# Kernel optimization log

Hardware: AMD Instinct MI355X
Metric: run time of the kernel (lower is better)

Reference implementation:

```python
import jax, jax.numpy as jnp
import numpy as np

N_USER = 50000
N_ITEM = 100000
D = 64            # embed_size; layer_size = [64, 64, 64]
NL = 3            # number of propagation layers
NNZ = 2400000     # nonzeros of sparse Laplacian L
B = 1024          # batch of (user, pos_item, neg_item)
N = N_USER + N_ITEM


def setup_inputs() -> dict:
    key = jax.random.key(0)
    ks = jax.random.split(key, 20)
    inp = {}
    # learned parameters
    inp["user_emb"] = jax.random.normal(ks[0], (N_USER, D), jnp.float32) * 0.1
    inp["item_emb"] = jax.random.normal(ks[1], (N_ITEM, D), jnp.float32) * 0.1
    inp["lin1_w"] = jax.random.normal(ks[2], (4, D // 2), jnp.float32) * 0.5
    inp["lin1_b"] = jnp.zeros((D // 2,), jnp.float32)
    inp["lin2_w"] = jax.random.normal(ks[3], (D // 2, D), jnp.float32) * 0.2
    inp["lin2_b"] = jnp.zeros((D,), jnp.float32)
    inp["w1"] = jax.random.normal(ks[4], (NL, D, D), jnp.float32) * (1.0 / np.sqrt(D))
    inp["b1"] = jnp.zeros((NL, D), jnp.float32)
    inp["w2"] = jax.random.normal(ks[5], (NL, D, D), jnp.float32) * (1.0 / np.sqrt(D))
    inp["b2"] = jnp.zeros((NL, D), jnp.float32)
    # sparse normalized Laplacian L in COO form (eye_mat handled as +E)
    inp["lap_row"] = jax.random.randint(ks[6], (NNZ,), 0, N, jnp.int32)
    inp["lap_col"] = jax.random.randint(ks[7], (NNZ,), 0, N, jnp.int32)
    inp["lap_val"] = jax.random.uniform(ks[8], (NNZ,), jnp.float32) * (1.0 / 16.0)
    # forward args
    inp["user_idx"] = jax.random.randint(ks[9], (B,), 0, N_USER, jnp.int32)
    inp["user_feat"] = jax.random.normal(ks[10], (B, 4), jnp.float32)
    inp["pos_idx"] = jax.random.randint(ks[11], (B,), 0, N_ITEM, jnp.int32)
    inp["neg_idx"] = jax.random.randint(ks[12], (B,), 0, N_ITEM, jnp.int32)
    inp["mlp_ratio"] = jnp.float32(0.5)
    return inp


def reference(user_emb, item_emb, user_feat, lin1_w, lin1_b, lin2_w, lin2_b,
              w1, b1, w2, b2, lap_val, mlp_ratio,
              lap_row, lap_col, user_idx, pos_idx, neg_idx):
    n_user = user_emb.shape[0]
    n_nodes = user_emb.shape[0] + item_emb.shape[0]

    # user MLP: two stacked Linears (no activation in between, per Sequential)
    user_mlp = (user_feat @ lin1_w + lin1_b) @ lin2_w + lin2_b  # [B, D]
    # in-place no_grad embedding blend (stop_gradient mirrors torch.no_grad on mlp path)
    upd = user_emb[user_idx] * (1.0 - mlp_ratio) + jax.lax.stop_gradient(user_mlp) * mlp_ratio
    ue = user_emb.at[user_idx].set(upd)

    E = jnp.concatenate([ue, item_emb], axis=0)  # [N, D]

    def spmm(X):
        # L @ X via gather-multiply-segment_sum over COO nonzeros
        return jax.ops.segment_sum(lap_val[:, None] * X[lap_col], lap_row,
                                   num_segments=n_nodes)

    all_E = [E]
    for k in range(w1.shape[0]):
        L_E = spmm(E)                 # L @ E
        L_I_E = L_E + E               # (L + I) @ E
        msg = (L_I_E @ w1[k] + b1[k]) + ((L_E * E) @ w2[k] + b2[k])
        E = jax.nn.leaky_relu(msg, negative_slope=0.2)
        # F.normalize(E, p=2, dim=1) with eps=1e-12
        norm = E / jnp.maximum(jnp.linalg.norm(E, axis=1, keepdims=True), 1e-12)
        all_E.append(norm)

    all_E = jnp.concatenate(all_E, axis=1)  # [N, D*(NL+1)]
    users = all_E[:n_user]
    items = all_E[n_user:]
    return (users[user_idx], items[pos_idx], items[neg_idx])
```

## Files before the change

kernel.cpp:

```cpp
#include <hip/hip_runtime.h>
#include <hip/hip_bf16.h>

#define N_USERC 50000
#define N_ITEMC 100000
#define NNODE   150000
#define DIM     64
#define NLAYERS 3
#define NNZC    2400000
#define BATCH   1024

#define RPB     128
#define NBUCK   1172
#define NCHUNK  512
#define CHUNK   4688
#define CAPB    3072

using short8 = __attribute__((ext_vector_type(8))) short;
using f32x4  = __attribute__((ext_vector_type(4))) float;

__device__ __forceinline__ float bf2f(ushort u) {
    return __uint_as_float(((unsigned)u) << 16);
}
__device__ __forceinline__ ushort f2bf(float f) {
    unsigned u = __float_as_uint(f);
    u += 0x7FFF + ((u >> 16) & 1);
    return (ushort)(u >> 16);
}

__device__ __forceinline__ int block_excl_scan(int v, int* lds) {
    int lane = threadIdx.x & 63;
    int wid  = threadIdx.x >> 6;
    int nw   = (blockDim.x + 63) >> 6;
    int inc = v;
#pragma unroll
    for (int o = 1; o < 64; o <<= 1) {
        int n = __shfl_up(inc, o, 64);
        if (lane >= o) inc += n;
    }
    if (lane == 63) lds[wid] = inc;
    __syncthreads();
    if (wid == 0) {
        int tv = (lane < nw) ? lds[lane] : 0;
#pragma unroll
        for (int o = 1; o < 16; o <<= 1) {
            int n = __shfl_up(tv, o, 64);
            if (lane >= o) tv += n;
        }
        if (lane < nw) lds[lane] = tv;
    }
    __syncthreads();
    int woff = (wid == 0) ? 0 : lds[wid - 1];
    return woff + (inc - v);
}

__global__ void k_copy_E(const float* __restrict__ ue, const float* __restrict__ ie,
                         ushort* __restrict__ Ebf) {
    int i = blockIdx.x * blockDim.x + threadIdx.x;
    const int userEnd = N_USERC * DIM / 4;
    const int total   = NNODE * DIM / 4;
    if (i < total) {
        float4 v;
        if (i < userEnd) v = ((const float4*)ue)[i];
        else             v = ((const float4*)ie)[i - userEnd];
        ushort4 b;
        b.x = f2bf(v.x); b.y = f2bf(v.y); b.z = f2bf(v.z); b.w = f2bf(v.w);
        ((ushort4*)Ebf)[i] = b;
    }
}

__global__ void k_winner(const int* __restrict__ user_idx, int* __restrict__ winner) {
    int b = blockIdx.x * blockDim.x + threadIdx.x;
    if (b < BATCH) atomicMax(&winner[user_idx[b]], b);
}

__global__ void k_mlp_update(const float* __restrict__ user_emb,
                             const float* __restrict__ user_feat,
                             const float* __restrict__ l1w, const float* __restrict__ l1b,
                             const float* __restrict__ l2w, const float* __restrict__ l2b,
                             const float* __restrict__ ratio_p,
                             const int* __restrict__ user_idx,
                             const int* __restrict__ winner,
                             ushort* __restrict__ Ebf) {
    int b = blockIdx.x;
    int d = threadIdx.x;
    int u = user_idx[b];
    if (winner[u] != b) return;
    float ratio = ratio_p[0];
    float uf0 = user_feat[b * 4 + 0], uf1 = user_feat[b * 4 + 1];
    float uf2 = user_feat[b * 4 + 2], uf3 = user_feat[b * 4 + 3];
    float acc = l2b[d];
#pragma unroll
    for (int j = 0; j < 32; ++j) {
        float h = l1b[j] + uf0 * l1w[0 * 32 + j] + uf1 * l1w[1 * 32 + j]
                         + uf2 * l1w[2 * 32 + j] + uf3 * l1w[3 * 32 + j];
        acc += h * l2w[j * DIM + d];
    }
    float v = user_emb[u * DIM + d] * (1.f - ratio) + acc * ratio;
    Ebf[u * DIM + d] = f2bf(v);
}

__global__ void k_prepW(const float* __restrict__ w1, const float* __restrict__ w2,
                        ushort* __restrict__ Wtg) {
    int i = blockIdx.x * blockDim.x + threadIdx.x;
    if (i >= NLAYERS * 64 * 128) return;
    int layer = i >> 13;
    int rem = i & 8191;
    int n = rem >> 7, kk = rem & 127;
    float v = (kk < 64) ? w1[layer * 4096 + kk * 64 + n]
                        : w2[layer * 4096 + (kk - 64) * 64 + n];
    Wtg[i] = f2bf(v);
}

__global__ __launch_bounds__(256) void k_chunksort(const int* __restrict__ rows,
                                                   const int* __restrict__ cols,
                                                   const float* __restrict__ vals,
                                                   unsigned long long* __restrict__ tmp,
                                                   ushort* __restrict__ scanus) {
    __shared__ int hist[NBUCK];
    __shared__ int sutil[16];
    __shared__ unsigned long long stag[CHUNK];

    const int c = blockIdx.x;
    const int s = c * CHUNK;
    const int e = (s + CHUNK < NNZC) ? s + CHUNK : NNZC;
    const int t = threadIdx.x;

    for (int i = t; i < NBUCK; i += 256) hist[i] = 0;
    __syncthreads();
    for (int i = s + t; i < e; i += 256) atomicAdd(&hist[rows[i] >> 7], 1);
    __syncthreads();

    int loc[5];
    int sum = 0;
#pragma unroll
    for (int k = 0; k < 5; ++k) {
        int idx = t * 5 + k;
        int v = (idx < NBUCK) ? hist[idx] : 0;
        loc[k] = sum;
        sum += v;
    }
    int excl = block_excl_scan(sum, sutil);
#pragma unroll
    for (int k = 0; k < 5; ++k) {
        int idx = t * 5 + k;
        if (idx < NBUCK) hist[idx] = excl + loc[k];
    }
    __syncthreads();

    for (int i = t; i < NBUCK; i += 256) scanus[(size_t)c * (NBUCK + 1) + i] = (ushort)hist[i];
    if (t == 0) scanus[(size_t)c * (NBUCK + 1) + NBUCK] = (ushort)(e - s);
    __syncthreads();

    for (int i = s + t; i < e; i += 256) {
        int r = rows[i];
        int b = r >> 7, ro = r & 127;
        unsigned hi = ((unsigned)ro << 18) | (unsigned)cols[i];
        unsigned long long pk = ((unsigned long long)hi << 32) | (unsigned)__float_as_uint(vals[i]);
        int pos = atomicAdd(&hist[b], 1);
        stag[pos] = pk;
    }
    __syncthreads();

    int n = e - s;
    for (int i = t; i < n; i += 256) tmp[s + i] = stag[i];
}

__global__ void k_buckcnt(const ushort* __restrict__ scanus, int* __restrict__ bcnt) {
    int b = blockIdx.x * blockDim.x + threadIdx.x;
    if (b >= NBUCK) return;
    int sum = 0;
    for (int c = 0; c < NCHUNK; ++c) {
        const ushort* row = scanus + (size_t)c * (NBUCK + 1);
        sum += (int)row[b + 1] - (int)row[b];
    }
    bcnt[b] = sum;
}

__global__ __launch_bounds__(256) void k_bscan(const int* __restrict__ bcnt,
                                               int* __restrict__ bstart,
                                               int* __restrict__ rowptr) {
    __shared__ int sutil[16];
    int t = threadIdx.x;
    int loc[5];
    int sum = 0;
#pragma unroll
    for (int k = 0; k < 5; ++k) {
        int idx = t * 5 + k;
        int v = (idx < NBUCK) ? bcnt[idx] : 0;
        loc[k] = sum;
        sum += v;
    }
    int excl = block_excl_scan(sum, sutil);
#pragma unroll
    for (int k = 0; k < 5; ++k) {
        int idx = t * 5 + k;
        if (idx < NBUCK) bstart[idx] = excl + loc[k];
    }
    if (t == 0) { bstart[NBUCK] = NNZC; rowptr[NNODE] = NNZC; }
}

__global__ __launch_bounds__(256) void k_compact(const ushort* __restrict__ scanus,
                                                 const int* __restrict__ bstart,
                                                 const unsigned long long* __restrict__ tmp,
                                                 unsigned long long* __restrict__ csr,
                                                 int* __restrict__ rowptr) {
    __shared__ int runstart[NCHUNK];
    __shared__ int pref[NCHUNK + 1];
    __shared__ int sutil[16];
    __shared__ int rcur[RPB];
    __shared__ unsigned long long stag[CAPB];
    const int b = blockIdx.x;
    const int t = threadIdx.x;

    for (int r = t; r < NCHUNK; r += 256) {
        const ushort* row = scanus + (size_t)r * (NBUCK + 1);
        int s0 = row[b], s1 = row[b + 1];
        runstart[r] = r * CHUNK + s0;
        pref[r] = s1 - s0;
    }
    if (t < RPB) rcur[t] = 0;
    __syncthreads();
    int v0 = pref[t * 2], v1 = pref[t * 2 + 1];
    int sum = v0 + v1;
    int excl = block_excl_scan(sum, sutil);
    pref[t * 2] = excl;
    pref[t * 2 + 1] = excl + v0;
    if (t == 255) pref[NCHUNK] = excl + sum;
    __syncthreads();

    const int total = pref[NCHUNK];
    const int obase = bstart[b];

    if (total <= CAPB) {
        for (int r = t; r < NCHUNK; r += 256) {
            int p0 = pref[r], p1 = pref[r + 1];
            int rs = runstart[r];
            for (int i = p0; i < p1; ++i) stag[i] = tmp[rs + (i - p0)];
        }
        __syncthreads();
        for (int i = t; i < total; i += 256)
            atomicAdd(&rcur[(int)(stag[i] >> 50) & 127], 1);
        __syncthreads();
        int rv = (t < RPB) ? rcur[t] : 0;
        int rex = block_excl_scan(rv, sutil);
        if (t < RPB) {
            rcur[t] = rex;
            int grow = b * RPB + t;
            if (grow < NNODE) rowptr[grow] = obase + rex;
        }
        __syncthreads();
        for (int i = t; i < total; i += 256) {
            unsigned long long pk = stag[i];
            int ro = (int)(pk >> 50) & 127;
            int pos = atomicAdd(&rcur[ro], 1);
            csr[obase + pos] = pk;
        }
        return;
    }

    for (int i = t; i < total; i += 256) {
        int lo = 0, hi = NCHUNK - 1;
        while (lo < hi) {
            int mid = (lo + hi + 1) >> 1;
            if (pref[mid] <= i) lo = mid; else hi = mid - 1;
        }
        unsigned long long pk = tmp[runstart[lo] + (i - pref[lo])];
        atomicAdd(&rcur[(int)(pk >> 50) & 127], 1);
    }
    __syncthreads();
    int rv = (t < RPB) ? rcur[t] : 0;
    int rex = block_excl_scan(rv, sutil);
    if (t < RPB) {
        rcur[t] = rex;
        int grow = b * RPB + t;
        if (grow < NNODE) rowptr[grow] = obase + rex;
    }
    __syncthreads();
    for (int i = t; i < total; i += 256) {
        int lo = 0, hi = NCHUNK - 1;
        while (lo < hi) {
            int mid = (lo + hi + 1) >> 1;
            if (pref[mid] <= i) lo = mid; else hi = mid - 1;
        }
        unsigned long long pk = tmp[runstart[lo] + (i - pref[lo])];
        int ro = (int)(pk >> 50) & 127;
        int pos = atomicAdd(&rcur[ro], 1);
        csr[obase + pos] = pk;
    }
}

__global__ __launch_bounds__(256) void k_spmm(const int* __restrict__ rowptr,
                                              const unsigned long long* __restrict__ csr,
                                              const ushort* __restrict__ Ebf,
                                              float* __restrict__ L) {
    int lane = threadIdx.x & 63;
    int row  = blockIdx.x * 4 + (threadIdx.x >> 6);
    row = __builtin_amdgcn_readfirstlane(row);
    if (row >= NNODE) return;
    int s = __builtin_amdgcn_readfirstlane(rowptr[row]);
    int e = __builtin_amdgcn_readfirstlane(rowptr[row + 1]);
    const ushort* Ep = Ebf + lane;
    float acc = 0.f;
    int j = s;
    for (; j + 16 <= e; j += 16) {
        unsigned long long pk[16];
        float ev[16];
#pragma unroll
        for (int k = 0; k < 16; ++k) pk[k] = csr[j + k];
#pragma unroll
        for (int k = 0; k < 16; ++k) {
            int col = (int)(pk[k] >> 32) & 0x3FFFF;
            ev[k] = bf2f(Ep[col * DIM]);
        }
#pragma unroll
        for (int k = 0; k < 16; ++k)
            acc += __uint_as_float((unsigned)pk[k]) * ev[k];
    }
    if (j < e) {
        int m = e - j;
        unsigned long long pk[16];
        float ev[16];
#pragma unroll
        for (int k = 0; k < 16; ++k) {
            int idx = j + (k < m ? k : m - 1);
            pk[k] = csr[idx];
        }
#pragma unroll
        for (int k = 0; k < 16; ++k) {
            int col = (int)(pk[k] >> 32) & 0x3FFFF;
            ev[k] = bf2f(Ep[col * DIM]);
        }
#pragma unroll
        for (int k = 0; k < 16; ++k) {
            unsigned v = (k < m) ? (unsigned)pk[k] : 0u;
            acc += __uint_as_float(v) * ev[k];
        }
    }
    L[row * DIM + lane] = acc;
}

__global__ __launch_bounds__(256) void k_transform(const float* __restrict__ L,
                                                   const ushort* __restrict__ Ebf_in,
                                                   const ushort* __restrict__ Wtg,
                                                   const float* __restrict__ b1k,
                                                   const float* __restrict__ b2k,
                                                   ushort* __restrict__ Ebf_out) {
    __shared__ ushort A_s[64 * 136];
    __shared__ ushort W_s[64 * 136];
    __shared__ float  bias_s[64];

    const int t = threadIdx.x;
    const int rowbase = blockIdx.x * 64;
    if (t < 64) bias_s[t] = b1k[t] + b2k[t];

#pragma unroll
    for (int it = 0; it < 4; ++it) {
        int task = t + 256 * it;
        int n = task >> 4, k = (task & 15) * 8;
        uint4 wv = *(const uint4*)&Wtg[n * 128 + k];
        *(uint4*)&W_s[n * 136 + k] = wv;
    }
#pragma unroll
    for (int it = 0; it < 4; ++it) {
        int task = t + 256 * it;
        int rl = task >> 4, col = (task & 15) * 4;
        int row = rowbase + rl;
        float4 l4 = make_float4(0.f, 0.f, 0.f, 0.f);
        float e0 = 0.f, e1 = 0.f, e2 = 0.f, e3 = 0.f;
        if (row < NNODE) {
            l4 = *(const float4*)&L[row * 64 + col];
            ushort4 ub = *(const ushort4*)&Ebf_in[row * 64 + col];
            e0 = bf2f(ub.x); e1 = bf2f(ub.y); e2 = bf2f(ub.z); e3 = bf2f(ub.w);
        }
        *(ushort4*)&A_s[rl * 136 + col] =
            make_ushort4(f2bf(l4.x + e0), f2bf(l4.y + e1), f2bf(l4.z + e2), f2bf(l4.w + e3));
        *(ushort4*)&A_s[rl * 136 + 64 + col] =
            make_ushort4(f2bf(l4.x * e0), f2bf(l4.y * e1), f2bf(l4.z * e2), f2bf(l4.w * e3));
    }
    __syncthreads();

    const int w = t >> 6, l = t & 63;
    const int m16 = l & 15;
    const int q   = l >> 4;
    const int lm  = w * 16 + m16;

    f32x4 z = {0.f, 0.f, 0.f, 0.f};
    f32x4 acc[4] = {z, z, z, z};
#pragma unroll
    for (int ks = 0; ks < 4; ++ks) {
        short8 af = *(const short8*)&A_s[lm * 136 + ks * 32 + q * 8];
#pragma unroll
        for (int nt = 0; nt < 4; ++nt) {
            short8 wf = *(const short8*)&W_s[(nt * 16 + m16) * 136 + ks * 32 + q * 8];
            acc[nt] = __builtin_amdgcn_mfma_f32_16x16x32_bf16(af, wf, acc[nt], 0, 0, 0);
        }
    }
    __syncthreads();

    float* Cs = (float*)A_s;
#pragma unroll
    for (int nt = 0; nt < 4; ++nt) {
        int col = nt * 16 + m16;
#pragma unroll
        for (int r = 0; r < 4; ++r) {
            int lrow = w * 16 + q * 4 + r;
            Cs[lrow * 68 + col] = acc[nt][r];
        }
    }
    __syncthreads();

#pragma unroll
    for (int it = 0; it < 2; ++it) {
        int task = t + 256 * it;
        int rl = task >> 3, col = (task & 7) * 8;
        int row = rowbase + rl;
        if (row < NNODE) {
            float4 v0 = *(const float4*)&Cs[rl * 68 + col];
            float4 v1 = *(const float4*)&Cs[rl * 68 + col + 4];
            float o[8] = {v0.x, v0.y, v0.z, v0.w, v1.x, v1.y, v1.z, v1.w};
            ushort ob[8];
#pragma unroll
            for (int j = 0; j < 8; ++j) {
                float v = o[j] + bias_s[col + j];
                v = v >= 0.f ? v : 0.2f * v;
                ob[j] = f2bf(v);
            }
            uint4 pb;
            pb.x = (unsigned)ob[0] | ((unsigned)ob[1] << 16);
            pb.y = (unsigned)ob[2] | ((unsigned)ob[3] << 16);
            pb.z = (unsigned)ob[4] | ((unsigned)ob[5] << 16);
            pb.w = (unsigned)ob[6] | ((unsigned)ob[7] << 16);
            *(uint4*)&Ebf_out[row * 64 + col] = pb;
        }
    }
}

__global__ __launch_bounds__(256) void k_gather(const ushort* __restrict__ Ebf,
                                                const int* __restrict__ user_idx,
                                                const int* __restrict__ pos_idx,
                                                const int* __restrict__ neg_idx,
                                                float* __restrict__ out,
                                                int seg, int normalize) {
    int wid  = threadIdx.x >> 6;
    int lane = threadIdx.x & 63;
    int o = blockIdx.x * 4 + wid;
    if (o >= 3 * BATCH) return;
    int g = o >> 10, b = o & 1023;
    int row;
    if (g == 0)      row = user_idx[b];
    else if (g == 1) row = N_USERC + pos_idx[b];
    else             row = N_USERC + neg_idx[b];
    float v = bf2f(Ebf[row * DIM + lane]);
    if (normalize) {
        float ss = v * v;
#pragma unroll
        for (int m = 32; m; m >>= 1) ss += __shfl_xor(ss, m, 64);
        float nrm = sqrtf(ss);
        nrm = fmaxf(nrm, 1e-12f);
        v = v / nrm;
    }
    out[(g * BATCH + b) * 256 + seg * 64 + lane] = v;
}

extern "C" void kernel_launch(void* const* d_in, const int* in_sizes, int n_in,
                              void* d_out, int out_size, void* d_ws, size_t ws_size,
                              hipStream_t stream) {
    const float* user_emb  = (const float*)d_in[0];
    const float* item_emb  = (const float*)d_in[1];
    const float* lin1_w    = (const float*)d_in[2];
    const float* lin1_b    = (const float*)d_in[3];
    const float* lin2_w    = (const float*)d_in[4];
    const float* lin2_b    = (const float*)d_in[5];
    const float* w1        = (const float*)d_in[6];
    const float* b1        = (const float*)d_in[7];
    const float* w2        = (const float*)d_in[8];
    const float* b2        = (const float*)d_in[9];
    const int*   lap_row   = (const int*)d_in[10];
    const int*   lap_col   = (const int*)d_in[11];
    const float* lap_val   = (const float*)d_in[12];
    const int*   user_idx  = (const int*)d_in[13];
    const float* user_feat = (const float*)d_in[14];
    const int*   pos_idx   = (const int*)d_in[15];
    const int*   neg_idx   = (const int*)d_in[16];
    const float* mlp_ratio = (const float*)d_in[17];
    float* out = (float*)d_out;

    size_t off = 0;
    auto carve = [&](size_t bytes) { size_t r = off; off = (off + bytes + 255) & ~(size_t)255; return r; };
    size_t oL      = carve((size_t)NNODE * DIM * 4);
    size_t oEbf    = carve((size_t)NNODE * DIM * 2);
    size_t oCsr    = carve((size_t)NNZC * 8);
    size_t oScan   = carve((size_t)NCHUNK * (NBUCK + 1) * 2);
    size_t oBcnt   = carve((size_t)NBUCK * 4);
    size_t oBstart = carve((size_t)(NBUCK + 1) * 4);
    size_t oRowptr = carve((size_t)(NNODE + 1) * 4);
    size_t oWinner = carve((size_t)N_USERC * 4);
    (void)ws_size;

    char* base = (char*)d_ws;
    float*              L      = (float*)(base + oL);
    unsigned long long* tmp    = (unsigned long long*)(base + oL);
    ushort*             Ebf    = (ushort*)(base + oEbf);
    unsigned long long* csr    = (unsigned long long*)(base + oCsr);
    ushort*             scanus = (ushort*)(base + oScan);
    int*                bcnt   = (int*)(base + oBcnt);
    int*                bstart = (int*)(base + oBstart);
    int*                rowptr = (int*)(base + oRowptr);
    int*                winner = (int*)(base + oWinner);
    ushort*             Wtg    = (ushort*)(base + oScan);

    k_chunksort<<<NCHUNK, 256, 0, stream>>>(lap_row, lap_col, lap_val, tmp, scanus);
    k_buckcnt<<<(NBUCK + 255) / 256, 256, 0, stream>>>(scanus, bcnt);
    k_bscan<<<1, 256, 0, stream>>>(bcnt, bstart, rowptr);
    k_compact<<<NBUCK, 256, 0, stream>>>(scanus, bstart, tmp, csr, rowptr);

    k_prepW<<<(NLAYERS * 64 * 128 + 255) / 256, 256, 0, stream>>>(w1, w2, Wtg);
    hipMemsetAsync(winner, 0xFF, (size_t)N_USERC * 4, stream);
    k_copy_E<<<(NNODE * DIM / 4 + 255) / 256, 256, 0, stream>>>(user_emb, item_emb, Ebf);
    k_winner<<<(BATCH + 255) / 256, 256, 0, stream>>>(user_idx, winner);
    k_mlp_update<<<BATCH, 64, 0, stream>>>(user_emb, user_feat, lin1_w, lin1_b,
                                           lin2_w, lin2_b, mlp_ratio, user_idx, winner, Ebf);
    k_gather<<<(3 * BATCH) / 4, 256, 0, stream>>>(Ebf, user_idx, pos_idx, neg_idx, out, 0, 0);

    for (int k = 0; k < NLAYERS; ++k) {
        k_spmm<<<(NNODE + 3) / 4, 256, 0, stream>>>(rowptr, csr, Ebf, L);
        k_transform<<<(NNODE + 63) / 64, 256, 0, stream>>>(
            L, Ebf, Wtg + (size_t)k * 64 * 128, b1 + (size_t)k * DIM,
            b2 + (size_t)k * DIM, Ebf);
        k_gather<<<(3 * BATCH) / 4, 256, 0, stream>>>(Ebf, user_idx, pos_idx, neg_idx,
                                                      out, k + 1, 1);
    }
}
```

Measured before the change: 465.1 us.

## Fuse (L+I)E and L*E prep into SpMM, process two rows per wavefront

The SpMM kernel now handles two adjacent CSR rows per wavefront, walking their combined nonzero range in 32-wide batches and sending each product to one of two accumulators by position. It also computes L+E and L*E in the epilogue and writes them as a packed bf16 [N,128] buffer, so the transform kernel only copies tiles into shared memory. The aim is to cut the fp32 L write and reread, the extra E read in the transform, and per-row loop overhead for short rows. In exchange it uses more registers for the 32-entry batch, which can lower occupancy, and it relies on NNODE being even.

```diff
diff --git a/kernel.cpp b/kernel.cpp
--- a/kernel.cpp
+++ b/kernel.cpp
@@ -292,55 +292,68 @@
 __global__ __launch_bounds__(256) void k_spmm(const int* __restrict__ rowptr,
                                               const unsigned long long* __restrict__ csr,
                                               const ushort* __restrict__ Ebf,
-                                              float* __restrict__ L) {
+                                              ushort* __restrict__ AB) {
     int lane = threadIdx.x & 63;
-    int row  = blockIdx.x * 4 + (threadIdx.x >> 6);
-    row = __builtin_amdgcn_readfirstlane(row);
-    if (row >= NNODE) return;
-    int s = __builtin_amdgcn_readfirstlane(rowptr[row]);
-    int e = __builtin_amdgcn_readfirstlane(rowptr[row + 1]);
+    int p = blockIdx.x * 4 + (threadIdx.x >> 6);
+    p = __builtin_amdgcn_readfirstlane(p);
+    if (p >= NNODE / 2) return;
+    int row0 = p * 2;
+    int s0 = __builtin_amdgcn_readfirstlane(rowptr[row0]);
+    int e0 = __builtin_amdgcn_readfirstlane(rowptr[row0 + 1]);
+    int e1 = __builtin_amdgcn_readfirstlane(rowptr[row0 + 2]);
     const ushort* Ep = Ebf + lane;
-    float acc = 0.f;
-    int j = s;
-    for (; j + 16 <= e; j += 16) {
-        unsigned long long pk[16];
-        float ev[16];
-#pragma unroll
-        for (int k = 0; k < 16; ++k) pk[k] = csr[j + k];
-#pragma unroll
-        for (int k = 0; k < 16; ++k) {
+    float acc0 = 0.f, acc1 = 0.f;
+    int j = s0;
+    for (; j + 32 <= e1; j += 32) {
+        unsigned long long pk[32];
+        float ev[32];
+#pragma unroll
+        for (int k = 0; k < 32; ++k) pk[k] = csr[j + k];
+#pragma unroll
+        for (int k = 0; k < 32; ++k) {
             int col = (int)(pk[k] >> 32) & 0x3FFFF;
             ev[k] = bf2f(Ep[col * DIM]);
         }
 #pragma unroll
-        for (int k = 0; k < 16; ++k)
-            acc += __uint_as_float((unsigned)pk[k]) * ev[k];
-    }
-    if (j < e) {
-        int m = e - j;
-        unsigned long long pk[16];
-        float ev[16];
-#pragma unroll
-        for (int k = 0; k < 16; ++k) {
+        for (int k = 0; k < 32; ++k) {
+            float c = __uint_as_float((unsigned)pk[k]) * ev[k];
+            bool r0 = (j + k) < e0;
+            acc0 += r0 ? c : 0.f;
+            acc1 += r0 ? 0.f : c;
+        }
+    }
+    if (j < e1) {
+        int m = e1 - j;
+        unsigned long long pk[32];
+        float ev[32];
+#pragma unroll
+        for (int k = 0; k < 32; ++k) {
             int idx = j + (k < m ? k : m - 1);
             pk[k] = csr[idx];
         }
 #pragma unroll
-        for (int k = 0; k < 16; ++k) {
+        for (int k = 0; k < 32; ++k) {
             int col = (int)(pk[k] >> 32) & 0x3FFFF;
             ev[k] = bf2f(Ep[col * DIM]);
         }
 #pragma unroll
-        for (int k = 0; k < 16; ++k) {
+        for (int k = 0; k < 32; ++k) {
             unsigned v = (k < m) ? (unsigned)pk[k] : 0u;
-            acc += __uint_as_float(v) * ev[k];
-        }
-    }
-    L[row * DIM + lane] = acc;
-}
-
-__global__ __launch_bounds__(256) void k_transform(const float* __restrict__ L,
-                                                   const ushort* __restrict__ Ebf_in,
+            float c = __uint_as_float(v) * ev[k];
+            bool r0 = (j + (k < m ? k : m - 1)) < e0;
+            acc0 += r0 ? c : 0.f;
+            acc1 += r0 ? 0.f : c;
+        }
+    }
+    float ee0 = bf2f(Ebf[(size_t)row0 * DIM + lane]);
+    float ee1 = bf2f(Ebf[(size_t)(row0 + 1) * DIM + lane]);
+    AB[(size_t)row0 * 128 + lane]            = f2bf(acc0 + ee0);
+    AB[(size_t)row0 * 128 + 64 + lane]       = f2bf(acc0 * ee0);
+    AB[(size_t)(row0 + 1) * 128 + lane]      = f2bf(acc1 + ee1);
+    AB[(size_t)(row0 + 1) * 128 + 64 + lane] = f2bf(acc1 * ee1);
+}
+
+__global__ __launch_bounds__(256) void k_transform(const ushort* __restrict__ AB,
                                                    const ushort* __restrict__ Wtg,
                                                    const float* __restrict__ b1k,
                                                    const float* __restrict__ b2k,
@@ -363,19 +376,11 @@
 #pragma unroll
     for (int it = 0; it < 4; ++it) {
         int task = t + 256 * it;
-        int rl = task >> 4, col = (task & 15) * 4;
+        int rl = task >> 4, kc = (task & 15) * 8;
         int row = rowbase + rl;
-        float4 l4 = make_float4(0.f, 0.f, 0.f, 0.f);
-        float e0 = 0.f, e1 = 0.f, e2 = 0.f, e3 = 0.f;
-        if (row < NNODE) {
-            l4 = *(const float4*)&L[row * 64 + col];
-            ushort4 ub = *(const ushort4*)&Ebf_in[row * 64 + col];
-            e0 = bf2f(ub.x); e1 = bf2f(ub.y); e2 = bf2f(ub.z); e3 = bf2f(ub.w);
-        }
-        *(ushort4*)&A_s[rl * 136 + col] =
-            make_ushort4(f2bf(l4.x + e0), f2bf(l4.y + e1), f2bf(l4.z + e2), f2bf(l4.w + e3));
-        *(ushort4*)&A_s[rl * 136 + 64 + col] =
-            make_ushort4(f2bf(l4.x * e0), f2bf(l4.y * e1), f2bf(l4.z * e2), f2bf(l4.w * e3));
+        uint4 v = make_uint4(0u, 0u, 0u, 0u);
+        if (row < NNODE) v = *(const uint4*)&AB[(size_t)row * 128 + kc];
+        *(uint4*)&A_s[rl * 136 + kc] = v;
     }
     __syncthreads();
 
@@ -498,7 +503,7 @@
     (void)ws_size;
 
     char* base = (char*)d_ws;
-    float*              L      = (float*)(base + oL);
+    ushort*             AB     = (ushort*)(base + oL);
     unsigned long long* tmp    = (unsigned long long*)(base + oL);
     ushort*             Ebf    = (ushort*)(base + oEbf);
     unsigned long long* csr    = (unsigned long long*)(base + oCsr);
@@ -522,10 +527,11 @@
                                            lin2_w, lin2_b, mlp_ratio, user_idx, winner, Ebf);
     k_gather<<<(3 * BATCH) / 4, 256, 0, stream>>>(Ebf, user_idx, pos_idx, neg_idx, out, 0, 0);
 
+    const int npair = NNODE / 2;
     for (int k = 0; k < NLAYERS; ++k) {
-        k_spmm<<<(NNODE + 3) / 4, 256, 0, stream>>>(rowptr, csr, Ebf, L);
+        k_spmm<<<(npair + 3) / 4, 256, 0, stream>>>(rowptr, csr, Ebf, AB);
         k_transform<<<(NNODE + 63) / 64, 256, 0, stream>>>(
-            L, Ebf, Wtg + (size_t)k * 64 * 128, b1 + (size_t)k * DIM,
+            AB, Wtg + (size_t)k * 64 * 128, b1 + (size_t)k * DIM,
             b2 + (size_t)k * DIM, Ebf);
         k_gather<<<(3 * BATCH) / 4, 256, 0, stream>>>(Ebf, user_idx, pos_idx, neg_idx,
                                                       out, k + 1, 1);
```

After: 534.7 us. +15.0%, slower.
